# Optimization experiments

Hardware: AMD Instinct MI355X
Metric: run time of the kernel (lower is better)

The kernel has to match this reference:

```python
import jax, jax.numpy as jnp
import numpy as np
from jax.scipy.linalg import solve_triangular

EPS = 2e-5

def setup_inputs() -> dict:
    key = jax.random.key(0)
    k1, k2 = jax.random.split(key)
    B, N, H, W = 8, 256, 128, 128
    cont_feat = jax.random.normal(k1, (B, N, H, W), dtype=jnp.float32)
    styl_feat = jax.random.normal(k2, (B, N, H, W), dtype=jnp.float32)
    return {"cont_feat": cont_feat, "styl_feat": styl_feat}

def _cov(x):
    # x: [B, N, L], already centered. Returns [B, N, N]
    L = x.shape[-1]
    c = jnp.einsum('bnl,bml->bnm', x, x) / (L - 1)
    # eps jitter for Cholesky stability (original retries with eps on failure)
    return c + EPS * jnp.eye(x.shape[1], dtype=x.dtype)

def reference(cont_feat, styl_feat):
    B, N, cH, cW = cont_feat.shape
    xc = cont_feat.reshape(B, N, -1)
    xs = styl_feat.reshape(B, N, -1)

    # whitening of content
    c_mean = jnp.mean(xc, axis=-1, keepdims=True)
    xc_c = xc - c_mean
    Lc = jnp.linalg.cholesky(_cov(xc_c))           # [B, N, N] lower
    whiten_c = solve_triangular(Lc, xc_c, lower=True)  # == inv(Lc) @ xc_c

    # coloring with style statistics
    s_mean = jnp.mean(xs, axis=-1, keepdims=True)
    xs_c = xs - s_mean
    Ls = jnp.linalg.cholesky(_cov(xs_c))
    color = jnp.einsum('bnm,bml->bnl', Ls, whiten_c) + s_mean

    return color.reshape(B, N, cH, cW)
```

## Files before the change

### kernel.cpp

```cpp
#include <hip/hip_runtime.h>


#define BATCH 8
#define NF    256
#define LSP   16384
#define EPS_J 2e-5f

typedef float f32x4  __attribute__((ext_vector_type(4)));
typedef short bf16x8 __attribute__((ext_vector_type(8)));
typedef short short4v __attribute__((ext_vector_type(4)));

__device__ __forceinline__ short f2bf(float f) {
    unsigned u = __float_as_uint(f);
    u = (u + 0x7FFFu + ((u >> 16) & 1u)) >> 16;
    return (short)u;
}
__device__ __forceinline__ float bf2f(short s) {
    return __uint_as_float(((unsigned)(unsigned short)s) << 16);
}

__global__ __launch_bounds__(1024) void k_cov(const float* __restrict__ cont,
                                              const float* __restrict__ styl,
                                              float* __restrict__ gram,
                                              float* __restrict__ rowsum) {
    const int kc = blockIdx.x;
    const int m  = blockIdx.y;
    const float* __restrict__ src = (m < BATCH)
        ? cont + (size_t)m * NF * LSP
        : styl + (size_t)(m - BATCH) * NF * LSP;

    __shared__ short lds[256][72];

    const int t    = threadIdx.x;
    const int lane = t & 63;
    const int w    = t >> 6;
    const int wi   = (w & 3) * 64;
    const int wj   = (w >> 2) * 64;
    const int fr   = t >> 4;
    const int fc   = (t & 15) * 4;

    f32x4 acc[4][4];
    #pragma unroll
    for (int i = 0; i < 4; ++i)
        #pragma unroll
        for (int j = 0; j < 4; ++j) { f32x4 z = {0.f,0.f,0.f,0.f}; acc[i][j] = z; }

    float rs[4] = {0.f, 0.f, 0.f, 0.f};

    const size_t kbase = (size_t)kc * 1024;
    float4 pre[4];
    #pragma unroll
    for (int j = 0; j < 4; ++j)
        pre[j] = *(const float4*)(src + (size_t)(fr + j * 64) * LSP + kbase + fc);

    for (int step = 0; step < 16; ++step) {
        __syncthreads();
        #pragma unroll
        for (int j = 0; j < 4; ++j) {
            float4 v = pre[j];
            rs[j] += v.x + v.y + v.z + v.w;
            short4v b4 = { f2bf(v.x), f2bf(v.y), f2bf(v.z), f2bf(v.w) };
            *(short4v*)&lds[fr + j * 64][fc] = b4;
        }
        __syncthreads();
        if (step < 15) {
            const size_t k0n = kbase + (size_t)(step + 1) * 64;
            #pragma unroll
            for (int j = 0; j < 4; ++j)
                pre[j] = *(const float4*)(src + (size_t)(fr + j * 64) * LSP + k0n + fc);
        }
        #pragma unroll
        for (int ks = 0; ks < 2; ++ks) {
            const int kk   = ks * 32 + (lane >> 4) * 8;
            const int rsel = lane & 15;
            bf16x8 af[4], bfv[4];
            #pragma unroll
            for (int mi = 0; mi < 4; ++mi)
                af[mi] = *(const bf16x8*)&lds[wi + mi * 16 + rsel][kk];
            #pragma unroll
            for (int nj = 0; nj < 4; ++nj)
                bfv[nj] = *(const bf16x8*)&lds[wj + nj * 16 + rsel][kk];
            #pragma unroll
            for (int mi = 0; mi < 4; ++mi)
                #pragma unroll
                for (int nj = 0; nj < 4; ++nj)
                    acc[mi][nj] = __builtin_amdgcn_mfma_f32_16x16x32_bf16(
                        af[mi], bfv[nj], acc[mi][nj], 0, 0, 0);
        }
    }

    float* rsm = rowsum + m * NF;
    #pragma unroll
    for (int j = 0; j < 4; ++j) {
        float v = rs[j];
        v += __shfl_xor(v, 1);
        v += __shfl_xor(v, 2);
        v += __shfl_xor(v, 4);
        v += __shfl_xor(v, 8);
        if ((lane & 15) == 0) atomicAdd(rsm + fr + j * 64, v);
    }

    float* g = gram + (size_t)m * NF * NF;
    const int rowb = (lane >> 4) * 4;
    const int colb = lane & 15;
    #pragma unroll
    for (int mi = 0; mi < 4; ++mi)
        #pragma unroll
        for (int nj = 0; nj < 4; ++nj) {
            const int row = wi + mi * 16 + rowb;
            const int col = wj + nj * 16 + colb;
            #pragma unroll
            for (int r = 0; r < 4; ++r)
                atomicAdd(g + (size_t)(row + r) * NF + col, acc[mi][nj][r]);
        }
}


__device__ __forceinline__ void load_split_frag(const float* Lt, int row, int jb,
                                                int lane, bf16x8& h, bf16x8& l) {
    const int koff = (lane >> 4) * 8;
    const int base = ((row * (row + 1)) >> 1) + jb + koff;
    #pragma unroll
    for (int u = 0; u < 8; ++u) {
        const float f = Lt[base + u];
        const short hh = f2bf(f);
        h[u] = hh;
        l[u] = f2bf(f - bf2f(hh));
    }
}

__device__ __forceinline__ void apply_tile(int tile, bf16x8 ph, bf16x8 pl,
                                           float* Lt, short (*Pb)[40],
                                           const short (*Whs)[40],
                                           const short (*Wls)[40],
                                           int jb, int R0, int lane) {
    const int r0   = (tile >> 1) * 16;
    const int c0   = (tile & 1) * 16;
    const int koff = (lane >> 4) * 8;
    bf16x8 wh = *(const bf16x8*)&Whs[c0 + (lane & 15)][koff];
    bf16x8 wl = *(const bf16x8*)&Wls[c0 + (lane & 15)][koff];
    f32x4 acc = {0.f, 0.f, 0.f, 0.f};
    acc = __builtin_amdgcn_mfma_f32_16x16x32_bf16(ph, wh, acc, 0, 0, 0);
    acc = __builtin_amdgcn_mfma_f32_16x16x32_bf16(pl, wh, acc, 0, 0, 0);
    acc = __builtin_amdgcn_mfma_f32_16x16x32_bf16(ph, wl, acc, 0, 0, 0);
    const int col  = c0 + (lane & 15);
    const int rowb = r0 + (lane >> 4) * 4;
    #pragma unroll
    for (int rg = 0; rg < 4; ++rg) {
        const int rr  = rowb + rg;
        const int row = R0 + rr;
        Lt[((row * (row + 1)) >> 1) + jb + col] = acc[rg];
        Pb[rr][col] = f2bf(acc[rg]);
    }
}

__global__ __launch_bounds__(1024) void k_chol(float* __restrict__ Lg_all,
                                               const float* __restrict__ rowsum,
                                               float* __restrict__ LcT_all,
                                               float* __restrict__ mean_all) {
    const int m = blockIdx.x;
    float* __restrict__ Lg  = Lg_all + (size_t)m * NF * NF;
    float* __restrict__ LcT = (m < BATCH) ? (LcT_all + (size_t)m * NF * NF) : nullptr;

    __shared__ float Lt[32896];
    __shared__ float Sm[NF];
    __shared__ float Db[32][36];
    __shared__ short Whs[32][40];
    __shared__ short Wls[32][40];
    __shared__ short Pb[224][40];

    const int t    = threadIdx.x;
    const int lane = t & 63;
    const int wv   = t >> 6;

    if (t < NF) {
        float s = rowsum[m * NF + t];
        Sm[t] = s;
        mean_all[m * NF + t] = s * (1.f / (float)LSP);
    }
    __syncthreads();

    const float invLn  = 1.f / (float)LSP;
    const float invLm1 = 1.f / (float)(LSP - 1);
    for (int idx = t; idx < NF * NF; idx += 1024) {
        const int r = idx >> 8, c = idx & 255;
        if (c <= r) {
            float v = (Lg[idx] - Sm[r] * Sm[c] * invLn) * invLm1;
            if (c == r) v += EPS_J;
            Lt[((r * (r + 1)) >> 1) + c] = v;
        }
    }
    __syncthreads();

    for (int jb = 0; jb < NF; jb += 32) {
        const int R0 = jb + 32;
        const int R  = NF - R0;
        const int nT = (R >> 4) * 2;

        bf16x8 ph0, pl0, ph1, pl1;
        int tw0 = -1, tw1 = -1;
        if (wv > 0) {
            const int tb = wv - 1;
            if (tb < nT) {
                tw0 = tb;
                load_split_frag(Lt, R0 + (tb >> 1) * 16 + (lane & 15), jb, lane, ph0, pl0);
            }
            if (tb + 15 < nT) {
                tw1 = tb + 15;
                load_split_frag(Lt, R0 + ((tb + 15) >> 1) * 16 + (lane & 15), jb, lane, ph1, pl1);
            }
        } else if (t < 32) {
            const int r = t;
            const int rbase = (((jb + r) * (jb + r + 1)) >> 1) + jb;
            float a[32];
            #pragma unroll
            for (int c = 0; c < 32; ++c)
                a[c] = (c <= r) ? Lt[rbase + c] : 0.f;
            #pragma unroll
            for (int j = 0; j < 32; ++j) {
                const float ajv = a[j];
                const float d   = __shfl(ajv, j);
                const float rd  = __builtin_amdgcn_rcpf(d);
                const float rs  = __builtin_amdgcn_rsqf(d);
                const float sc  = ajv * rd;
                #pragma unroll
                for (int c = j + 1; c < 32; ++c)
                    a[c] -= sc * __shfl(ajv, c);
                a[j] = ajv * rs;
            }
            #pragma unroll
            for (int c = 0; c < 32; ++c)
                if (c <= r) Lt[rbase + c] = a[c];
            #pragma unroll
            for (int c4 = 0; c4 < 8; ++c4) {
                f32x4 v = { a[c4 * 4], a[c4 * 4 + 1], a[c4 * 4 + 2], a[c4 * 4 + 3] };
                *(f32x4*)&Db[r][c4 * 4] = v;
            }

            if (R > 0) {
                const int k = r;
                float wcol[32];
                #pragma unroll
                for (int c = 0; c < 32; ++c) wcol[c] = 0.f;
                #pragma unroll
                for (int c = 0; c < 32; ++c) {
                    float s = (c == k) ? 1.f : 0.f;
                    const int ng = c >> 2;
                    #pragma unroll
                    for (int g = 0; g <= 7; ++g) {
                        if (g <= ng) {
                            f32x4 dv = *(const f32x4*)&Db[c][g * 4];
                            s -= dv[0] * wcol[g * 4]     + dv[1] * wcol[g * 4 + 1]
                               + dv[2] * wcol[g * 4 + 2] + dv[3] * wcol[g * 4 + 3];
                        }
                    }
                    wcol[c] = s * __builtin_amdgcn_rcpf(Db[c][c]);
                }
                #pragma unroll
                for (int c = 0; c < 32; ++c) {
                    const float wv_ = wcol[c];
                    const short hh = f2bf(wv_);
                    Whs[c][k] = hh;
                    Wls[c][k] = f2bf(wv_ - bf2f(hh));
                }
            }
        }
        __syncthreads();

        if (tw0 >= 0) apply_tile(tw0, ph0, pl0, Lt, Pb, Whs, Wls, jb, R0, lane);
        if (tw1 >= 0) apply_tile(tw1, ph1, pl1, Lt, Pb, Whs, Wls, jb, R0, lane);
        __syncthreads();

        if (R > 0) {
            const int nt  = R >> 4;
            const int ntt = nt * (nt + 1) / 2;
            for (int tt = wv; tt < ntt; tt += 16) {
                int tr = (int)((sqrtf(8.f * (float)tt + 1.f) - 1.f) * 0.5f);
                while ((tr + 1) * (tr + 2) / 2 <= tt) ++tr;
                while (tr * (tr + 1) / 2 > tt) --tr;
                const int tc = tt - tr * (tr + 1) / 2;
                const int r0 = tr * 16, c0 = tc * 16;
                bf16x8 af  = *(const bf16x8*)&Pb[r0 + (lane & 15)][(lane >> 4) * 8];
                bf16x8 bfv = *(const bf16x8*)&Pb[c0 + (lane & 15)][(lane >> 4) * 8];
                f32x4 accv = {0.f, 0.f, 0.f, 0.f};
                accv = __builtin_amdgcn_mfma_f32_16x16x32_bf16(af, bfv, accv, 0, 0, 0);
                const int col  = R0 + c0 + (lane & 15);
                const int rowb = R0 + r0 + (lane >> 4) * 4;
                if (tr != tc) {
                    #pragma unroll
                    for (int rg = 0; rg < 4; ++rg) {
                        const int row = rowb + rg;
                        Lt[((row * (row + 1)) >> 1) + col] -= accv[rg];
                    }
                } else {
                    #pragma unroll
                    for (int rg = 0; rg < 4; ++rg) {
                        const int row = rowb + rg;
                        if (col <= row)
                            Lt[((row * (row + 1)) >> 1) + col] -= accv[rg];
                    }
                }
            }
        }
        __syncthreads();
    }

    if (LcT) {
        for (int idx = t; idx < NF * NF; idx += 1024) {
            const int cc = idx >> 8, rr = idx & 255;
            if (rr >= cc) LcT[idx] = Lt[((rr * (rr + 1)) >> 1) + cc];
        }
    } else {
        for (int idx = t; idx < NF * NF; idx += 1024) {
            const int r = idx >> 8, c = idx & 255;
            if (c <= r) Lg[idx] = Lt[((r * (r + 1)) >> 1) + c];
        }
    }
}

__global__ __launch_bounds__(256) void k_solveT(const float* __restrict__ Lg_all,
                                                const float* __restrict__ LcT_all,
                                                const float* __restrict__ mean_all,
                                                short* __restrict__ Tbf,
                                                float* __restrict__ bias) {
    const int lane = threadIdx.x & 63;
    const int wv   = threadIdx.x >> 6;
    const int task = blockIdx.x * 4 + wv;
    const int b    = task >> 8;
    const int i    = task & 255;
    const float* __restrict__ Ls  = Lg_all + (size_t)(BATCH + b) * NF * NF + (size_t)i * NF;
    const float* __restrict__ LcT = LcT_all + (size_t)b * NF * NF;

    __shared__ float vbuf[4][NF];
    float* vb = vbuf[wv];
    for (int k = lane; k < NF; k += 64) vb[k] = 0.f;

    int j = i;
    for (; j >= 1; j -= 2) {
        const float* __restrict__ r0 = LcT + (size_t)j * NF;
        const float* __restrict__ r1 = r0 - NF;
        float s0 = 0.f, s1 = 0.f;
        for (int k = j + 1 + lane; k <= i; k += 64) {
            const float tk = vb[k];
            s0 += tk * r0[k];
            s1 += tk * r1[k];
        }
        #pragma unroll
        for (int mm = 32; mm >= 1; mm >>= 1) {
            s0 += __shfl_xor(s0, mm);
            s1 += __shfl_xor(s1, mm);
        }
        if (lane == 0) {
            const float tj  = (Ls[j] - s0) / r0[j];
            const float tjm = (Ls[j - 1] - s1 - tj * r1[j]) / r1[j - 1];
            vb[j]     = tj;
            vb[j - 1] = tjm;
        }
    }
    if (j == 0) {
        const float* __restrict__ r0 = LcT;
        float s0 = 0.f;
        for (int k = 1 + lane; k <= i; k += 64) s0 += vb[k] * r0[k];
        #pragma unroll
        for (int mm = 32; mm >= 1; mm >>= 1) s0 += __shfl_xor(s0, mm);
        if (lane == 0) vb[0] = (Ls[0] - s0) / r0[0];
    }

    const float* __restrict__ cm  = mean_all + b * NF;
    const float* __restrict__ smn = mean_all + (BATCH + b) * NF;
    float dot = 0.f;
    for (int k = lane; k < NF; k += 64) dot += vb[k] * cm[k];
    #pragma unroll
    for (int mm = 32; mm >= 1; mm >>= 1) dot += __shfl_xor(dot, mm);
    if (lane == 0) bias[b * NF + i] = smn[i] - dot;

    short* __restrict__ Tr = Tbf + (size_t)b * NF * NF + (size_t)i * NF;
    const int k4 = lane * 4;
    short4v o = { f2bf(vb[k4]), f2bf(vb[k4 + 1]), f2bf(vb[k4 + 2]), f2bf(vb[k4 + 3]) };
    *(short4v*)&Tr[k4] = o;
}

__global__ __launch_bounds__(256) void k_out(const float* __restrict__ cont,
                                             const short* __restrict__ Tbf,
                                             const float* __restrict__ bias,
                                             float* __restrict__ out) {
    const int b  = blockIdx.y;
    const int l0 = blockIdx.x * 64;
    const float* __restrict__ X  = cont + (size_t)b * NF * LSP;
    const short* __restrict__ Tb = Tbf + (size_t)b * NF * NF;
    float* __restrict__ O = out + (size_t)b * NF * LSP;

    __shared__ short a_s[256][72];
    __shared__ short b_s[64][72];
    __shared__ float bias_s[NF];

    const int t    = threadIdx.x;
    const int lane = t & 63;
    const int w    = t >> 6;

    bias_s[t] = bias[b * NF + t];

    f32x4 acc[4][4];
    #pragma unroll
    for (int i = 0; i < 4; ++i)
        #pragma unroll
        for (int j = 0; j < 4; ++j) { f32x4 z = {0.f,0.f,0.f,0.f}; acc[i][j] = z; }

    const int kb = (t >> 4) * 4;
    const int lb = (t & 15) * 4;
    const int fr = t >> 4;
    const int fc = (t & 15) * 4;

    float4 xr[4];
    #pragma unroll
    for (int r = 0; r < 4; ++r)
        xr[r] = *(const float4*)(X + (size_t)(kb + r) * LSP + l0 + lb);

    for (int step = 0; step < 4; ++step) {
        const int k0 = step * 64;
        __syncthreads();
        #pragma unroll
        for (int s2 = 0; s2 < 16; ++s2) {
            const int row = fr + s2 * 16;
            *(short4v*)&a_s[row][fc] = *(const short4v*)(Tb + (size_t)row * NF + k0 + fc);
        }
        {
            short4v c0v = { f2bf(xr[0].x), f2bf(xr[1].x), f2bf(xr[2].x), f2bf(xr[3].x) };
            short4v c1v = { f2bf(xr[0].y), f2bf(xr[1].y), f2bf(xr[2].y), f2bf(xr[3].y) };
            short4v c2v = { f2bf(xr[0].z), f2bf(xr[1].z), f2bf(xr[2].z), f2bf(xr[3].z) };
            short4v c3v = { f2bf(xr[0].w), f2bf(xr[1].w), f2bf(xr[2].w), f2bf(xr[3].w) };
            *(short4v*)&b_s[lb + 0][kb] = c0v;
            *(short4v*)&b_s[lb + 1][kb] = c1v;
            *(short4v*)&b_s[lb + 2][kb] = c2v;
            *(short4v*)&b_s[lb + 3][kb] = c3v;
        }
        __syncthreads();
        if (step < 3) {
            const int k0n = k0 + 64;
            #pragma unroll
            for (int r = 0; r < 4; ++r)
                xr[r] = *(const float4*)(X + (size_t)(k0n + kb + r) * LSP + l0 + lb);
        }
        #pragma unroll
        for (int ks = 0; ks < 2; ++ks) {
            const int kk   = ks * 32 + (lane >> 4) * 8;
            const int rsel = lane & 15;
            bf16x8 af[4], bfv[4];
            #pragma unroll
            for (int mi = 0; mi < 4; ++mi)
                af[mi] = *(const bf16x8*)&a_s[w * 64 + mi * 16 + rsel][kk];
            #pragma unroll
            for (int nj = 0; nj < 4; ++nj)
                bfv[nj] = *(const bf16x8*)&b_s[nj * 16 + rsel][kk];
            #pragma unroll
            for (int mi = 0; mi < 4; ++mi)
                #pragma unroll
                for (int nj = 0; nj < 4; ++nj)
                    acc[mi][nj] = __builtin_amdgcn_mfma_f32_16x16x32_bf16(
                        af[mi], bfv[nj], acc[mi][nj], 0, 0, 0);
        }
    }

    #pragma unroll
    for (int mi = 0; mi < 4; ++mi) {
        const int row = w * 64 + mi * 16 + (lane >> 4) * 4;
        #pragma unroll
        for (int nj = 0; nj < 4; ++nj) {
            const int col = l0 + nj * 16 + (lane & 15);
            #pragma unroll
            for (int r = 0; r < 4; ++r)
                O[(size_t)(row + r) * LSP + col] = acc[mi][nj][r] + bias_s[row + r];
        }
    }
}

extern "C" void kernel_launch(void* const* d_in, const int* in_sizes, int n_in,
                              void* d_out, int out_size, void* d_ws, size_t ws_size,
                              hipStream_t stream) {
    (void)in_sizes; (void)n_in; (void)out_size; (void)ws_size;
    const float* cont = (const float*)d_in[0];
    const float* styl = (const float*)d_in[1];
    float* out = (float*)d_out;

    float* ws       = (float*)d_ws;
    float* gram     = ws;
    float* rowsum   = gram + 16 * 65536;
    float* mean_all = rowsum + 4096;
    float* bias     = mean_all + 4096;
    float* LcT      = bias + 2048;
    short* Tbf      = (short*)(LcT + 8 * 65536);

    hipMemsetAsync(gram, 0, (size_t)(16 * 65536 + 4096) * sizeof(float), stream);

    k_cov   <<<dim3(16, 16), 1024, 0, stream>>>(cont, styl, gram, rowsum);
    k_chol  <<<16,           1024, 0, stream>>>(gram, rowsum, LcT, mean_all);
    k_solveT<<<512,          256,  0, stream>>>(gram, LcT, mean_all, Tbf, bias);
    k_out   <<<dim3(256, 8), 256,  0, stream>>>(cont, Tbf, bias, out);
}
```

Before: 720.5 us.

## Compute only lower-triangle Gram tiles and replace atomics with split-K partial reduction

The covariance kernel now has only 10 of 16 waves compute the lower-triangular 64x64 tiles of the symmetric Gram matrix; the other six waves just load data. When the workspace is large enough, each block writes its partial tile to a scratch buffer, and a new reduce kernel sums the 16 K-splits deterministically instead of using float atomics. This removes redundant MFMA work and atomic contention, at the cost of an extra kernel launch and about 42MB of extra scratch traffic. Launch bounds hints were also added to two kernels.

```diff
diff --git a/kernel.cpp b/kernel.cpp
--- a/kernel.cpp
+++ b/kernel.cpp
@@ -19,10 +19,17 @@
     return __uint_as_float(((unsigned)(unsigned short)s) << 16);
 }
 
-__global__ __launch_bounds__(1024) void k_cov(const float* __restrict__ cont,
-                                              const float* __restrict__ styl,
-                                              float* __restrict__ gram,
-                                              float* __restrict__ rowsum) {
+__device__ __forceinline__ void tri_map(int w, int& ti, int& tj) {
+    ti = (w >= 6) ? 3 : ((w >= 3) ? 2 : ((w >= 1) ? 1 : 0));
+    tj = w - ti * (ti + 1) / 2;
+}
+
+__global__ __launch_bounds__(1024, 4) void k_cov(const float* __restrict__ cont,
+                                                 const float* __restrict__ styl,
+                                                 float* __restrict__ gram,
+                                                 float* __restrict__ rowsum,
+                                                 float* __restrict__ part,
+                                                 int use_part) {
     const int kc = blockIdx.x;
     const int m  = blockIdx.y;
     const float* __restrict__ src = (m < BATCH)
@@ -34,10 +41,12 @@
     const int t    = threadIdx.x;
     const int lane = t & 63;
     const int w    = t >> 6;
-    const int wi   = (w & 3) * 64;
-    const int wj   = (w >> 2) * 64;
-    const int fr   = t >> 4;
-    const int fc   = (t & 15) * 4;
+    int ti = 0, tj = 0;
+    tri_map(w < 10 ? w : 0, ti, tj);
+    const int wi = ti * 64;
+    const int wj = tj * 64;
+    const int fr = t >> 4;
+    const int fc = (t & 15) * 4;
 
     f32x4 acc[4][4];
     #pragma unroll
@@ -69,23 +78,25 @@
             for (int j = 0; j < 4; ++j)
                 pre[j] = *(const float4*)(src + (size_t)(fr + j * 64) * LSP + k0n + fc);
         }
-        #pragma unroll
-        for (int ks = 0; ks < 2; ++ks) {
-            const int kk   = ks * 32 + (lane >> 4) * 8;
-            const int rsel = lane & 15;
-            bf16x8 af[4], bfv[4];
-            #pragma unroll
-            for (int mi = 0; mi < 4; ++mi)
-                af[mi] = *(const bf16x8*)&lds[wi + mi * 16 + rsel][kk];
-            #pragma unroll
-            for (int nj = 0; nj < 4; ++nj)
-                bfv[nj] = *(const bf16x8*)&lds[wj + nj * 16 + rsel][kk];
-            #pragma unroll
-            for (int mi = 0; mi < 4; ++mi)
+        if (w < 10) {
+            #pragma unroll
+            for (int ks = 0; ks < 2; ++ks) {
+                const int kk   = ks * 32 + (lane >> 4) * 8;
+                const int rsel = lane & 15;
+                bf16x8 af[4], bfv[4];
+                #pragma unroll
+                for (int mi = 0; mi < 4; ++mi)
+                    af[mi] = *(const bf16x8*)&lds[wi + mi * 16 + rsel][kk];
                 #pragma unroll
                 for (int nj = 0; nj < 4; ++nj)
-                    acc[mi][nj] = __builtin_amdgcn_mfma_f32_16x16x32_bf16(
-                        af[mi], bfv[nj], acc[mi][nj], 0, 0, 0);
+                    bfv[nj] = *(const bf16x8*)&lds[wj + nj * 16 + rsel][kk];
+                #pragma unroll
+                for (int mi = 0; mi < 4; ++mi)
+                    #pragma unroll
+                    for (int nj = 0; nj < 4; ++nj)
+                        acc[mi][nj] = __builtin_amdgcn_mfma_f32_16x16x32_bf16(
+                            af[mi], bfv[nj], acc[mi][nj], 0, 0, 0);
+            }
         }
     }
 
@@ -100,19 +111,52 @@
         if ((lane & 15) == 0) atomicAdd(rsm + fr + j * 64, v);
     }
 
-    float* g = gram + (size_t)m * NF * NF;
+    if (w >= 10) return;
+
     const int rowb = (lane >> 4) * 4;
     const int colb = lane & 15;
-    #pragma unroll
-    for (int mi = 0; mi < 4; ++mi)
-        #pragma unroll
-        for (int nj = 0; nj < 4; ++nj) {
-            const int row = wi + mi * 16 + rowb;
-            const int col = wj + nj * 16 + colb;
-            #pragma unroll
-            for (int r = 0; r < 4; ++r)
-                atomicAdd(g + (size_t)(row + r) * NF + col, acc[mi][nj][r]);
-        }
+    if (use_part) {
+        float* __restrict__ pt = part + (((size_t)m * 16 + kc) * 10 + w) * 4096;
+        #pragma unroll
+        for (int mi = 0; mi < 4; ++mi)
+            #pragma unroll
+            for (int nj = 0; nj < 4; ++nj) {
+                const int rl = mi * 16 + rowb;
+                const int cl = nj * 16 + colb;
+                #pragma unroll
+                for (int r = 0; r < 4; ++r)
+                    pt[(size_t)(rl + r) * 64 + cl] = acc[mi][nj][r];
+            }
+    } else {
+        float* g = gram + (size_t)m * NF * NF;
+        #pragma unroll
+        for (int mi = 0; mi < 4; ++mi)
+            #pragma unroll
+            for (int nj = 0; nj < 4; ++nj) {
+                const int row = wi + mi * 16 + rowb;
+                const int col = wj + nj * 16 + colb;
+                #pragma unroll
+                for (int r = 0; r < 4; ++r)
+                    atomicAdd(g + (size_t)(row + r) * NF + col, acc[mi][nj][r]);
+            }
+    }
+}
+
+__global__ __launch_bounds__(256) void k_reduce(const float* __restrict__ part,
+                                                float* __restrict__ gram) {
+    const int m  = blockIdx.x / 10;
+    const int tt = blockIdx.x % 10;
+    int ti, tj;
+    tri_map(tt, ti, tj);
+    const float* __restrict__ base = part + ((size_t)m * 16 * 10 + tt) * 4096;
+    float* __restrict__ g = gram + (size_t)m * NF * NF;
+    for (int e = threadIdx.x; e < 4096; e += 256) {
+        float s = 0.f;
+        #pragma unroll
+        for (int sp = 0; sp < 16; ++sp)
+            s += base[(size_t)sp * 10 * 4096 + e];
+        g[(size_t)(ti * 64 + (e >> 6)) * NF + tj * 64 + (e & 63)] = s;
+    }
 }
 
 
@@ -154,10 +198,10 @@
     }
 }
 
-__global__ __launch_bounds__(1024) void k_chol(float* __restrict__ Lg_all,
-                                               const float* __restrict__ rowsum,
-                                               float* __restrict__ LcT_all,
-                                               float* __restrict__ mean_all) {
+__global__ __launch_bounds__(1024, 4) void k_chol(float* __restrict__ Lg_all,
+                                                  const float* __restrict__ rowsum,
+                                                  float* __restrict__ LcT_all,
+                                                  float* __restrict__ mean_all) {
     const int m = blockIdx.x;
     float* __restrict__ Lg  = Lg_all + (size_t)m * NF * NF;
     float* __restrict__ LcT = (m < BATCH) ? (LcT_all + (size_t)m * NF * NF) : nullptr;
@@ -477,7 +521,7 @@
 extern "C" void kernel_launch(void* const* d_in, const int* in_sizes, int n_in,
                               void* d_out, int out_size, void* d_ws, size_t ws_size,
                               hipStream_t stream) {
-    (void)in_sizes; (void)n_in; (void)out_size; (void)ws_size;
+    (void)in_sizes; (void)n_in; (void)out_size;
     const float* cont = (const float*)d_in[0];
     const float* styl = (const float*)d_in[1];
     float* out = (float*)d_out;
@@ -489,10 +533,21 @@
     float* bias     = mean_all + 4096;
     float* LcT      = bias + 2048;
     short* Tbf      = (short*)(LcT + 8 * 65536);
-
-    hipMemsetAsync(gram, 0, (size_t)(16 * 65536 + 4096) * sizeof(float), stream);
-
-    k_cov   <<<dim3(16, 16), 1024, 0, stream>>>(cont, styl, gram, rowsum);
+    float* part     = (float*)(Tbf + 8 * 65536);
+
+    const size_t need = ((size_t)((char*)(part + (size_t)16 * 16 * 10 * 4096)
+                                  - (char*)ws));
+    const int use_part = (ws_size >= need) ? 1 : 0;
+
+    if (use_part) {
+        hipMemsetAsync(rowsum, 0, (size_t)4096 * sizeof(float), stream);
+    } else {
+        hipMemsetAsync(gram, 0, (size_t)(16 * 65536 + 4096) * sizeof(float), stream);
+    }
+
+    k_cov   <<<dim3(16, 16), 1024, 0, stream>>>(cont, styl, gram, rowsum, part, use_part);
+    if (use_part)
+        k_reduce<<<160, 256, 0, stream>>>(part, gram);
     k_chol  <<<16,           1024, 0, stream>>>(gram, rowsum, LcT, mean_all);
     k_solveT<<<512,          256,  0, stream>>>(gram, LcT, mean_all, Tbf, bias);
     k_out   <<<dim3(256, 8), 256,  0, stream>>>(cont, Tbf, bias, out);
```

Result: faster. 698.6 us (-3.0%).
